# Kernel optimization log

Measured on AMD Instinct MI355X. Metric: run time of the kernel, lower is better.

Reference implementation:

```python
import jax, jax.numpy as jnp
import numpy as np

EPS_NORM = 1e-8   # matches torch F.normalize default-ish eps used in cosine_dist
CLAMP_MIN = 1e-12
CLAMP_MAX = 1e12

def setup_inputs() -> dict:
    key = jax.random.key(0)
    k1, k2, k3 = jax.random.split(key, 3)
    N, D, C = 262144, 256, 64
    ref_emb = jax.random.normal(k1, (N, D), dtype=jnp.float32)
    ref_label = jax.random.randint(k2, (N,), 0, C)
    centers = jax.random.normal(k3, (C, D), dtype=jnp.float32)
    return {"ref_emb": ref_emb, "ref_label": ref_label, "centers": centers}

def reference(ref_emb, ref_label, centers):
    # center[i] = centers[ref_label[i]]  -> [N, D] gather
    center = centers[ref_label]
    # diag of pairwise cosine-distance matrix == row-wise cosine distance
    # cos_dist_i = 1 - <x_i, c_i> / (||x_i|| * ||c_i||)
    dot = jnp.sum(ref_emb * center, axis=-1)                     # [N]
    nx = jnp.sqrt(jnp.sum(ref_emb * ref_emb, axis=-1))           # [N]
    nc = jnp.sqrt(jnp.sum(center * center, axis=-1))             # [N]
    cos_sim = dot / jnp.maximum(nx * nc, EPS_NORM)
    cos_diag = 1.0 - cos_sim
    return jnp.mean(jnp.clip(cos_diag, CLAMP_MIN, CLAMP_MAX), axis=-1)
```

## Files before the change

kernel.cpp:

```cpp
#include <hip/hip_runtime.h>
#include <math.h>

constexpr int N = 262144;
constexpr int D = 256;
constexpr int C = 64;
constexpr float EPS_NORM  = 1e-8f;
constexpr float CLAMP_MIN = 1e-12f;
constexpr float CLAMP_MAX = 1e12f;

constexpr int BLOCKS = 2048;

__global__ __launch_bounds__(64) void center_norm_kernel(
        const float* __restrict__ centers, float* __restrict__ cnorm) {
    const int c = blockIdx.x;
    const int lane = threadIdx.x;
    float4 v = reinterpret_cast<const float4*>(centers + c * D)[lane];
    float s = v.x * v.x + v.y * v.y + v.z * v.z + v.w * v.w;
    #pragma unroll
    for (int off = 32; off >= 1; off >>= 1)
        s += __shfl_xor(s, off, 64);
    if (lane == 0) cnorm[c] = sqrtf(s);
}

__global__ __launch_bounds__(256) void inner_cos_kernel(
        const float* __restrict__ emb,
        const int*   __restrict__ label,
        const float* __restrict__ centers,
        const float* __restrict__ cnorm,
        float* __restrict__ partials) {
    const int lane = threadIdx.x & 63;
    const int wave = threadIdx.x >> 6;
    const int sub  = lane & 15;
    const int quad = lane >> 4;
    const int gwave   = (blockIdx.x << 2) | wave;
    const int ngroups = N >> 2;
    const int nwave   = BLOCKS << 2;

    float lsum = 0.0f;
    for (int g = gwave; g < ngroups; g += nwave) {
        const int row = (g << 2) | quad;
        const int lab = label[row];
        const float4* xrow = reinterpret_cast<const float4*>(emb + (size_t)row * D);
        const float4* crow = reinterpret_cast<const float4*>(centers + (size_t)lab * D);

        float dot = 0.0f, nx2 = 0.0f;
        #pragma unroll
        for (int j = 0; j < 4; ++j) {
            const float4 x = xrow[(j << 4) + sub];
            const float4 c = crow[(j << 4) + sub];
            dot = fmaf(x.x, c.x, dot); dot = fmaf(x.y, c.y, dot);
            dot = fmaf(x.z, c.z, dot); dot = fmaf(x.w, c.w, dot);
            nx2 = fmaf(x.x, x.x, nx2); nx2 = fmaf(x.y, x.y, nx2);
            nx2 = fmaf(x.z, x.z, nx2); nx2 = fmaf(x.w, x.w, nx2);
        }
        #pragma unroll
        for (int off = 8; off >= 1; off >>= 1) {
            dot += __shfl_xor(dot, off, 64);
            nx2 += __shfl_xor(nx2, off, 64);
        }
        const float denom = fmaxf(sqrtf(nx2) * cnorm[lab], EPS_NORM);
        float cd = 1.0f - dot / denom;
        cd = fminf(fmaxf(cd, CLAMP_MIN), CLAMP_MAX);
        lsum += cd;
    }

    lsum += __shfl_xor(lsum, 16, 64);
    lsum += __shfl_xor(lsum, 32, 64);

    __shared__ float ssum[4];
    if (lane == 0) ssum[wave] = lsum;
    __syncthreads();
    if (threadIdx.x == 0)
        partials[blockIdx.x] = (ssum[0] + ssum[1]) + (ssum[2] + ssum[3]);
}

__global__ __launch_bounds__(256) void finalize_kernel(
        const float* __restrict__ partials, float* __restrict__ out) {
    float s = 0.0f;
    #pragma unroll
    for (int i = 0; i < BLOCKS / 256; ++i)
        s += partials[threadIdx.x + (i << 8)];
    #pragma unroll
    for (int off = 32; off >= 1; off >>= 1)
        s += __shfl_xor(s, off, 64);
    __shared__ float ss[4];
    if ((threadIdx.x & 63) == 0) ss[threadIdx.x >> 6] = s;
    __syncthreads();
    if (threadIdx.x == 0)
        out[0] = ((ss[0] + ss[1]) + (ss[2] + ss[3])) * (1.0f / (float)N);
}

extern "C" void kernel_launch(void* const* d_in, const int* in_sizes, int n_in,
                              void* d_out, int out_size, void* d_ws, size_t ws_size,
                              hipStream_t stream) {
    const float* emb     = (const float*)d_in[0];
    const int*   label   = (const int*)d_in[1];
    const float* centers = (const float*)d_in[2];
    float* out      = (float*)d_out;
    float* cnorm    = (float*)d_ws;
    float* partials = (float*)d_ws + 64;

    center_norm_kernel<<<C, 64, 0, stream>>>(centers, cnorm);
    inner_cos_kernel<<<BLOCKS, 256, 0, stream>>>(emb, label, centers, cnorm, partials);
    finalize_kernel<<<1, 256, 0, stream>>>(partials, out);
}
```

Before: 358.3 us.

## Prefetch next row group, preload labels, use pre-normalized centers

```diff
diff --git a/kernel.cpp b/kernel.cpp
--- a/kernel.cpp
+++ b/kernel.cpp
@@ -4,14 +4,15 @@
 constexpr int N = 262144;
 constexpr int D = 256;
 constexpr int C = 64;
-constexpr float EPS_NORM  = 1e-8f;
 constexpr float CLAMP_MIN = 1e-12f;
 constexpr float CLAMP_MAX = 1e12f;
 
 constexpr int BLOCKS = 2048;
+constexpr int NWAVES = BLOCKS * 4;
+constexpr int GPW    = (N / 4) / NWAVES;
 
-__global__ __launch_bounds__(64) void center_norm_kernel(
-        const float* __restrict__ centers, float* __restrict__ cnorm) {
+__global__ __launch_bounds__(64) void center_normalize_kernel(
+        const float* __restrict__ centers, float* __restrict__ cn) {
     const int c = blockIdx.x;
     const int lane = threadIdx.x;
     float4 v = reinterpret_cast<const float4*>(centers + c * D)[lane];
@@ -19,49 +20,76 @@
     #pragma unroll
     for (int off = 32; off >= 1; off >>= 1)
         s += __shfl_xor(s, off, 64);
-    if (lane == 0) cnorm[c] = sqrtf(s);
+    const float inv = rsqrtf(fmaxf(s, 1e-24f));
+    float4 o = make_float4(v.x * inv, v.y * inv, v.z * inv, v.w * inv);
+    reinterpret_cast<float4*>(cn + c * D)[lane] = o;
 }
 
 __global__ __launch_bounds__(256) void inner_cos_kernel(
         const float* __restrict__ emb,
         const int*   __restrict__ label,
-        const float* __restrict__ centers,
-        const float* __restrict__ cnorm,
+        const float* __restrict__ cnormed,
         float* __restrict__ partials) {
     const int lane = threadIdx.x & 63;
     const int wave = threadIdx.x >> 6;
     const int sub  = lane & 15;
     const int quad = lane >> 4;
-    const int gwave   = (blockIdx.x << 2) | wave;
-    const int ngroups = N >> 2;
-    const int nwave   = BLOCKS << 2;
+    const int gwave = (blockIdx.x << 2) | wave;
+
+    int mylab = 0;
+    if (lane < 32) {
+        const int k = lane >> 2, q = lane & 3;
+        mylab = label[4 * gwave + k * (4 * NWAVES) + q];
+    }
+
+    const float4* xbase = reinterpret_cast<const float4*>(emb);
+    const float4* cbase = reinterpret_cast<const float4*>(cnormed);
 
     float lsum = 0.0f;
-    for (int g = gwave; g < ngroups; g += nwave) {
-        const int row = (g << 2) | quad;
-        const int lab = label[row];
-        const float4* xrow = reinterpret_cast<const float4*>(emb + (size_t)row * D);
-        const float4* crow = reinterpret_cast<const float4*>(centers + (size_t)lab * D);
+    float4 x[4], c[4];
+
+    {
+        const int lab  = __shfl(mylab, quad);
+        const int row0 = 4 * gwave + quad;
+        const float4* xr = xbase + (size_t)row0 * (D / 4);
+        const float4* cr = cbase + (size_t)lab  * (D / 4);
+        #pragma unroll
+        for (int j = 0; j < 4; ++j) { x[j] = xr[(j << 4) + sub]; c[j] = cr[(j << 4) + sub]; }
+    }
+
+    #pragma unroll
+    for (int k = 0; k < GPW; ++k) {
+        float4 xn[4], cn[4];
+        if (k + 1 < GPW) {
+            const int labn = __shfl(mylab, ((k + 1) << 2) + quad);
+            const int rown = 4 * gwave + (k + 1) * (4 * NWAVES) + quad;
+            const float4* xr = xbase + (size_t)rown * (D / 4);
+            const float4* cr = cbase + (size_t)labn * (D / 4);
+            #pragma unroll
+            for (int j = 0; j < 4; ++j) { xn[j] = xr[(j << 4) + sub]; cn[j] = cr[(j << 4) + sub]; }
+        }
 
         float dot = 0.0f, nx2 = 0.0f;
         #pragma unroll
         for (int j = 0; j < 4; ++j) {
-            const float4 x = xrow[(j << 4) + sub];
-            const float4 c = crow[(j << 4) + sub];
-            dot = fmaf(x.x, c.x, dot); dot = fmaf(x.y, c.y, dot);
-            dot = fmaf(x.z, c.z, dot); dot = fmaf(x.w, c.w, dot);
-            nx2 = fmaf(x.x, x.x, nx2); nx2 = fmaf(x.y, x.y, nx2);
-            nx2 = fmaf(x.z, x.z, nx2); nx2 = fmaf(x.w, x.w, nx2);
+            dot = fmaf(x[j].x, c[j].x, dot); dot = fmaf(x[j].y, c[j].y, dot);
+            dot = fmaf(x[j].z, c[j].z, dot); dot = fmaf(x[j].w, c[j].w, dot);
+            nx2 = fmaf(x[j].x, x[j].x, nx2); nx2 = fmaf(x[j].y, x[j].y, nx2);
+            nx2 = fmaf(x[j].z, x[j].z, nx2); nx2 = fmaf(x[j].w, x[j].w, nx2);
         }
         #pragma unroll
         for (int off = 8; off >= 1; off >>= 1) {
             dot += __shfl_xor(dot, off, 64);
             nx2 += __shfl_xor(nx2, off, 64);
         }
-        const float denom = fmaxf(sqrtf(nx2) * cnorm[lab], EPS_NORM);
-        float cd = 1.0f - dot / denom;
+        float cd = 1.0f - dot * rsqrtf(fmaxf(nx2, 1e-24f));
         cd = fminf(fmaxf(cd, CLAMP_MIN), CLAMP_MAX);
         lsum += cd;
+
+        if (k + 1 < GPW) {
+            #pragma unroll
+            for (int j = 0; j < 4; ++j) { x[j] = xn[j]; c[j] = cn[j]; }
+        }
     }
 
     lsum += __shfl_xor(lsum, 16, 64);
@@ -97,10 +125,10 @@
     const int*   label   = (const int*)d_in[1];
     const float* centers = (const float*)d_in[2];
     float* out      = (float*)d_out;
-    float* cnorm    = (float*)d_ws;
-    float* partials = (float*)d_ws + 64;
+    float* cnormed  = (float*)d_ws;
+    float* partials = (float*)d_ws + C * D;
 
-    center_norm_kernel<<<C, 64, 0, stream>>>(centers, cnorm);
-    inner_cos_kernel<<<BLOCKS, 256, 0, stream>>>(emb, label, centers, cnorm, partials);
+    center_normalize_kernel<<<C, 64, 0, stream>>>(centers, cnormed);
+    inner_cos_kernel<<<BLOCKS, 256, 0, stream>>>(emb, label, cnormed, partials);
     finalize_kernel<<<1, 256, 0, stream>>>(partials, out);
 }
```

New measurement: 357.4 us. No clear change (-0.3%).
